# Optimization experiments

Measured on AMD Instinct MI355X. Metric: run time of the kernel, lower is better.

Reference implementation:

```python
import jax, jax.numpy as jnp
import numpy as np

N = 50000      # nodes
E = 800000     # edges
D = 128        # in_channels
H = 128        # hidden_channels
G = 64         # graphs in batch
OUT = 10       # out_channels
L = 6          # gcn layers (hardcoded in module)
EPS = 1e-5     # batchnorm eps


def setup_inputs() -> dict:
    key = jax.random.key(0)
    ks = jax.random.split(key, 8)
    s = 1.0 / np.sqrt(H)
    return {
        "x": jax.random.normal(ks[0], (N, D), jnp.float32),
        "edge_index": jax.random.randint(ks[1], (2, E), 0, N),
        "batch": jnp.sort(jax.random.randint(ks[2], (N,), 0, G)),
        "conv_W": jax.random.normal(ks[3], (L, D, H), jnp.float32) * s,
        "conv_b": jnp.zeros((L, H), jnp.float32),
        "bn_gamma": jnp.ones((L - 1, H), jnp.float32),
        "bn_beta": jnp.zeros((L - 1, H), jnp.float32),
        "head_W1": jax.random.normal(ks[4], (H, H), jnp.float32) * s,
        "head_b1": jnp.zeros((H,), jnp.float32),
        "head_bn_gamma": jnp.ones((H,), jnp.float32),
        "head_bn_beta": jnp.zeros((H,), jnp.float32),
        "head_W2": jax.random.normal(ks[5], (H, H), jnp.float32) * s,
        "head_b2": jnp.zeros((H,), jnp.float32),
        "head_W3": jax.random.normal(ks[6], (H, OUT), jnp.float32) * s,
        "head_b3": jnp.zeros((OUT,), jnp.float32),
    }


def _batchnorm(h, gamma, beta):
    # track_running_stats=False -> always batch statistics, biased variance
    mu = h.mean(axis=0)
    var = jnp.mean((h - mu) ** 2, axis=0)
    return (h - mu) * jax.lax.rsqrt(var + EPS) * gamma + beta


def reference(x, edge_index, batch, conv_W, conv_b, bn_gamma, bn_beta,
              head_W1, head_b1, head_bn_gamma, head_bn_beta,
              head_W2, head_b2, head_W3, head_b3):
    src, dst = edge_index[0], edge_index[1]
    # GCN symmetric norm with self-loops: deg = in-degree + 1
    deg = jnp.zeros((N,), x.dtype).at[dst].add(1.0) + 1.0
    dinv = jax.lax.rsqrt(deg)                 # deg^{-1/2}
    enorm = (dinv[src] * dinv[dst])[:, None]  # [E,1] edge weights
    self_w = (dinv * dinv)[:, None]           # [N,1] self-loop weight = 1/deg

    h = x
    for i in range(L):
        h = h @ conv_W[i]                                     # [N,H]
        agg = jnp.zeros_like(h).at[dst].add(h[src] * enorm)   # scatter-add
        h = agg + h * self_w + conv_b[i]
        if i < L - 1:
            h = jax.nn.relu(_batchnorm(h, bn_gamma[i], bn_beta[i]))
            # dropout(p=0.1) -> identity in eval

    # global_mean_pool over graphs
    counts = jnp.zeros((G,), h.dtype).at[batch].add(1.0)
    pooled = jnp.zeros((G, H), h.dtype).at[batch].add(h)
    pooled = pooled / jnp.clip(counts, 1.0)[:, None]

    # prediction head: Linear -> BN -> ReLU -> (Dropout) -> Linear -> ReLU -> Linear
    z = pooled @ head_W1 + head_b1
    z = jax.nn.relu(_batchnorm(z, head_bn_gamma, head_bn_beta))
    z = jax.nn.relu(z @ head_W2 + head_b2)
    return z @ head_W3 + head_b3
```

## Files before the change

### kernel.cpp

```cpp
#include <hip/hip_runtime.h>

#define N 50000
#define E 800000
#define H 128
#define G 64
#define OUTC 10
#define L 6
#define EPS 1e-5f
#define SLOTS 64

typedef unsigned short ushort_t;
typedef __attribute__((ext_vector_type(8))) short short8;
typedef __attribute__((ext_vector_type(8))) unsigned short ushort8;
typedef __attribute__((ext_vector_type(4))) float floatx4;

__device__ __forceinline__ void atomAddF(float* p, float v) {
  unsafeAtomicAdd(p, v);
}

__device__ __forceinline__ unsigned short f2bf(float f) {
  unsigned u = __float_as_uint(f);
  unsigned r = (u + 0x7FFF + ((u >> 16) & 1)) >> 16;
  return (unsigned short)r;
}
__device__ __forceinline__ float bf2f(unsigned short b) {
  return __uint_as_float(((unsigned)b) << 16);
}

__global__ void zero_kernel(int* __restrict__ p, int n) {
  int i = blockIdx.x * blockDim.x + threadIdx.x;
  if (i < n) p[i] = 0;
}

__global__ void csr_fill_kernel(const int* __restrict__ src, const int* __restrict__ dst,
                                int* __restrict__ cnt, int* __restrict__ csr) {
  int e = blockIdx.x * blockDim.x + threadIdx.x;
  if (e < E) {
    int d = dst[e];
    int pos = atomicAdd(&cnt[d], 1);
    if (pos < SLOTS) csr[(d << 6) + pos] = src[e];
  }
}

__global__ void dinv_kernel(const int* __restrict__ cnt, float* __restrict__ dinv) {
  int n = blockIdx.x * blockDim.x + threadIdx.x;
  if (n < N) dinv[n] = rsqrtf((float)(cnt[n] + 1));
}

__global__ void prep_kernel(const float* __restrict__ convW, ushort_t* __restrict__ WT) {
  int j = blockIdx.x * 256 + threadIdx.x;
  if (j < L * H * H) {
    int l = j >> 14, r = j & 16383;
    int n = r >> 7, k = r & 127;
    WT[j] = f2bf(convW[l * 16384 + k * 128 + n]);
  }
}

__global__ void cnt_kernel(const int* __restrict__ batch, float* __restrict__ cntg) {
  __shared__ int lb[G + 1];
  int t = threadIdx.x;
  if (t <= G) {
    int lo = 0, hi = N;
    while (lo < hi) { int m = (lo + hi) >> 1; if (batch[m] < t) lo = m + 1; else hi = m; }
    lb[t] = lo;
  }
  __syncthreads();
  if (t < G) cntg[t] = (float)(lb[t + 1] - lb[t]);
}

__global__ __launch_bounds__(256) void gemm_mfma_kernel(
    const ushort_t* __restrict__ Ab, const float* __restrict__ Af,
    const ushort_t* __restrict__ WT,
    const float* __restrict__ dinv, ushort_t* __restrict__ hWs,
    const float* __restrict__ bnsums, const float* __restrict__ gamma,
    const float* __restrict__ beta)
{
  const int tid = threadIdx.x;
  const int wave = tid >> 6, lane = tid & 63;
  const int quad = lane >> 4, m = lane & 15;
  const int row0 = blockIdx.x * 64 + wave * 16;
  const int arow = min(row0 + m, N - 1);
  const float invN = 1.0f / (float)N;

  short8 afrag[4];
  if (Af) {
#pragma unroll
    for (int kc = 0; kc < 4; ++kc) {
      const float* p = &Af[arow * H + kc * 32 + quad * 8];
      float4 f0 = *(const float4*)p;
      float4 f1 = *(const float4*)(p + 4);
      short8 a;
      a[0] = (short)f2bf(f0.x); a[1] = (short)f2bf(f0.y);
      a[2] = (short)f2bf(f0.z); a[3] = (short)f2bf(f0.w);
      a[4] = (short)f2bf(f1.x); a[5] = (short)f2bf(f1.y);
      a[6] = (short)f2bf(f1.z); a[7] = (short)f2bf(f1.w);
      afrag[kc] = a;
    }
  } else {
#pragma unroll
    for (int kc = 0; kc < 4; ++kc) {
      ushort8 raw = *(const ushort8*)&Ab[arow * H + kc * 32 + quad * 8];
      if (bnsums) {
        const int k0 = kc * 32 + quad * 8;
#pragma unroll
        for (int j = 0; j < 8; ++j) {
          float s = bnsums[k0 + j], q = bnsums[128 + k0 + j];
          float mu = s * invN;
          float var = q * invN - mu * mu;
          float rs = rsqrtf(var + EPS);
          float sc = gamma[k0 + j] * rs;
          float sh = beta[k0 + j] - mu * sc;
          raw[j] = f2bf(fmaxf(bf2f(raw[j]) * sc + sh, 0.f));
        }
      }
      short8 a;
#pragma unroll
      for (int j = 0; j < 8; ++j) a[j] = (short)raw[j];
      afrag[kc] = a;
    }
  }

  float dv[4];
#pragma unroll
  for (int i = 0; i < 4; ++i) {
    int r = row0 + quad * 4 + i;
    dv[i] = (r < N) ? dinv[r] : 0.f;
  }

  const short* WTs = (const short*)WT;
#pragma unroll
  for (int nt = 0; nt < 8; ++nt) {
    floatx4 acc = {0.f, 0.f, 0.f, 0.f};
#pragma unroll
    for (int kc = 0; kc < 4; ++kc) {
      short8 bfrag = *(const short8*)&WTs[(nt * 16 + m) * H + kc * 32 + quad * 8];
      acc = __builtin_amdgcn_mfma_f32_16x16x32_bf16(afrag[kc], bfrag, acc, 0, 0, 0);
    }
    int col = nt * 16 + m;
#pragma unroll
    for (int i = 0; i < 4; ++i) {
      int r = row0 + quad * 4 + i;
      if (r < N) hWs[r * H + col] = f2bf(acc[i] * dv[i]);
    }
  }
}

__global__ __launch_bounds__(256) void gather_kernel(
    const ushort_t* __restrict__ hWs, const int* __restrict__ csr,
    const int* __restrict__ cnt, const float* __restrict__ dinv,
    const float* __restrict__ bias, ushort_t* __restrict__ aggb)
{
  int t = blockIdx.x * 256 + threadIdx.x;
  int n = t >> 4, c8 = (t & 15) * 8;

  ushort8 us = *(const ushort8*)&hWs[n * H + c8];
  float acc[8];
#pragma unroll
  for (int j = 0; j < 8; ++j) acc[j] = bf2f(us[j]);

  int e = n << 6;
  int end = e + min(cnt[n], SLOTS);
  for (; e + 3 < end; e += 4) {
    int s0 = csr[e], s1 = csr[e + 1], s2 = csr[e + 2], s3 = csr[e + 3];
    ushort8 u0 = *(const ushort8*)&hWs[s0 * H + c8];
    ushort8 u1 = *(const ushort8*)&hWs[s1 * H + c8];
    ushort8 u2 = *(const ushort8*)&hWs[s2 * H + c8];
    ushort8 u3 = *(const ushort8*)&hWs[s3 * H + c8];
#pragma unroll
    for (int j = 0; j < 8; ++j)
      acc[j] += (bf2f(u0[j]) + bf2f(u1[j])) + (bf2f(u2[j]) + bf2f(u3[j]));
  }
  for (; e < end; ++e) {
    int s0 = csr[e];
    ushort8 u0 = *(const ushort8*)&hWs[s0 * H + c8];
#pragma unroll
    for (int j = 0; j < 8; ++j) acc[j] += bf2f(u0[j]);
  }

  float dn = dinv[n];
  float4 b0 = *(const float4*)&bias[c8];
  float4 b1 = *(const float4*)&bias[c8 + 4];
  float bb[8] = {b0.x, b0.y, b0.z, b0.w, b1.x, b1.y, b1.z, b1.w};
  ushort8 o;
#pragma unroll
  for (int j = 0; j < 8; ++j) o[j] = f2bf(acc[j] * dn + bb[j]);
  *(ushort8*)&aggb[n * H + c8] = o;
}

__global__ __launch_bounds__(256) void bn_stats_kernel(
    const ushort_t* __restrict__ a, float* __restrict__ sums)
{
  __shared__ float red[256];
  int tid = threadIdx.x;
  int c = tid & 127, half = tid >> 7;
  int r0 = blockIdx.x * 128;
  float s = 0.f, q = 0.f;
  for (int i = 0; i < 64; ++i) {
    int r = r0 + i * 2 + half;
    if (r < N) { float v = bf2f(a[r * H + c]); s += v; q += v * v; }
  }
  red[tid] = s; __syncthreads();
  float s2 = (half == 0) ? s + red[tid + 128] : 0.f;
  __syncthreads();
  red[tid] = q; __syncthreads();
  if (half == 0) {
    float q2 = q + red[tid + 128];
    atomAddF(&sums[c], s2);
    atomAddF(&sums[128 + c], q2);
  }
}

__global__ __launch_bounds__(256) void pool_kernel(
    const ushort_t* __restrict__ h, const int* __restrict__ batch,
    float* __restrict__ pooled )
{
  int r0 = blockIdx.x * 128;
  int rend = min(r0 + 128, N);
  int c = threadIdx.x & 127, half = threadIdx.x >> 7;
  float acc = 0.f;
  int curg = -1;
  for (int r = r0 + half; r < rend; r += 2) {
    int g = batch[r];
    if (g != curg) {
      if (curg >= 0) atomAddF(&pooled[curg * H + c], acc);
      acc = 0.f; curg = g;
    }
    acc += bf2f(h[r * H + c]);
  }
  if (curg >= 0) atomAddF(&pooled[curg * H + c], acc);
}

__global__ void head1_kernel(const float* __restrict__ pooled, const float* __restrict__ cntg,
                             const float* __restrict__ W1, const float* __restrict__ b1,
                             float* __restrict__ z1)
{
  int t = blockIdx.x * 256 + threadIdx.x;
  int g = t >> 7, c = t & 127;
  float s = 0.f;
  for (int k = 0; k < H; ++k) s += pooled[g * H + k] * W1[k * H + c];
  z1[t] = s / fmaxf(cntg[g], 1.0f) + b1[c];
}

__global__ void head_bn_kernel(float* __restrict__ z1,
                               const float* __restrict__ gamma, const float* __restrict__ beta)
{
  int c = threadIdx.x;
  float s = 0.f, q = 0.f;
  for (int g = 0; g < G; ++g) { float v = z1[g * H + c]; s += v; q += v * v; }
  float mu = s / (float)G;
  float var = q / (float)G - mu * mu;
  float rs = rsqrtf(var + EPS);
  float ga = gamma[c], be = beta[c];
  for (int g = 0; g < G; ++g) {
    float v = z1[g * H + c];
    z1[g * H + c] = fmaxf((v - mu) * rs * ga + be, 0.f);
  }
}

__global__ void head2_kernel(const float* __restrict__ z1, const float* __restrict__ W2,
                             const float* __restrict__ b2, float* __restrict__ z2)
{
  int t = blockIdx.x * 256 + threadIdx.x;
  int g = t >> 7, c = t & 127;
  float s = b2[c];
  for (int k = 0; k < H; ++k) s += z1[g * H + k] * W2[k * H + c];
  z2[t] = fmaxf(s, 0.f);
}

__global__ void head3_kernel(const float* __restrict__ z2, const float* __restrict__ W3,
                             const float* __restrict__ b3, float* __restrict__ out)
{
  int t = blockIdx.x * 256 + threadIdx.x;
  if (t < G * OUTC) {
    int g = t / OUTC, o = t % OUTC;
    float s = b3[o];
    for (int k = 0; k < H; ++k) s += z2[g * H + k] * W3[k * OUTC + o];
    out[t] = s;
  }
}

extern "C" void kernel_launch(void* const* d_in, const int* in_sizes, int n_in,
                              void* d_out, int out_size, void* d_ws, size_t ws_size,
                              hipStream_t stream) {
  const float* x     = (const float*)d_in[0];
  const int*   ei    = (const int*)d_in[1];
  const int*   srcp  = ei;
  const int*   dstp  = ei + E;
  const int*   batch = (const int*)d_in[2];
  const float* convW = (const float*)d_in[3];
  const float* convb = (const float*)d_in[4];
  const float* bng   = (const float*)d_in[5];
  const float* bnb   = (const float*)d_in[6];
  const float* W1    = (const float*)d_in[7];
  const float* b1    = (const float*)d_in[8];
  const float* hg    = (const float*)d_in[9];
  const float* hb    = (const float*)d_in[10];
  const float* W2    = (const float*)d_in[11];
  const float* b2    = (const float*)d_in[12];
  const float* W3    = (const float*)d_in[13];
  const float* b3    = (const float*)d_in[14];
  float* out = (float*)d_out;

  const size_t NH2 = (size_t)N * H / 2;
  float*    ws     = (float*)d_ws;
  ushort_t* aggb   = (ushort_t*)ws;
  ushort_t* hWs    = (ushort_t*)(ws + NH2);
  ushort_t* WT     = (ushort_t*)(ws + 2 * NH2);
  float*    dinv   = ws + 2 * NH2 + (L * H * H / 2);
  int*      csr    = (int*)(dinv + N);
  int*      cnt    = csr + (size_t)N * SLOTS;
  float*    bnsums = (float*)(cnt + N);
  float*    pooled = bnsums + (L - 1) * 256;
  float*    cntg   = pooled + G * H;
  float*    z1     = cntg + G;
  float*    z2     = z1 + G * H;

  const int zero_words = N + (L - 1) * 256 + G * H;
  zero_kernel<<<(zero_words + 255) / 256, 256, 0, stream>>>(cnt, zero_words);
  csr_fill_kernel<<<(E + 255) / 256, 256, 0, stream>>>(srcp, dstp, cnt, csr);
  dinv_kernel<<<(N + 255) / 256, 256, 0, stream>>>(cnt, dinv);
  cnt_kernel<<<1, 128, 0, stream>>>(batch, cntg);
  prep_kernel<<<(L * H * H + 255) / 256, 256, 0, stream>>>(convW, WT);

  for (int l = 0; l < L; ++l) {
    const ushort_t* Ab = (l == 0) ? nullptr : aggb;
    const float*    Af = (l == 0) ? x : nullptr;
    const float* bs = (l == 0) ? nullptr : bnsums + (l - 1) * 256;
    const float* ga = (l == 0) ? nullptr : bng + (size_t)(l - 1) * H;
    const float* be = (l == 0) ? nullptr : bnb + (size_t)(l - 1) * H;
    gemm_mfma_kernel<<<(N + 63) / 64, 256, 0, stream>>>(
        Ab, Af, WT + (size_t)l * H * H, dinv, hWs, bs, ga, be);
    gather_kernel<<<N * 16 / 256, 256, 0, stream>>>(
        hWs, csr, cnt, dinv, convb + (size_t)l * H, aggb);
    if (l < L - 1)
      bn_stats_kernel<<<(N + 127) / 128, 256, 0, stream>>>(aggb, bnsums + l * 256);
  }

  pool_kernel<<<(N + 127) / 128, 256, 0, stream>>>(aggb, batch, pooled);
  head1_kernel<<<32, 256, 0, stream>>>(pooled, cntg, W1, b1, z1);
  head_bn_kernel<<<1, 128, 0, stream>>>(z1, hg, hb);
  head2_kernel<<<32, 256, 0, stream>>>(z1, W2, b2, z2);
  head3_kernel<<<3, 256, 0, stream>>>(z2, W3, b3, out);
}
```

Measured before the change: 655.3 us.

## Store CSR indices as 16-bit, unroll gather by 8, vectorize BN stats

Neighbor indices are stored as unsigned 16-bit values, halving the CSR footprint, and the gather reads eight at once with a single vector load, issuing eight row fetches per iteration for more memory-level parallelism. The BN statistics kernel now reads 8 bf16 values per thread with vector loads and reduces across lanes with wave shuffles before a small shared-memory reduction. The 16-bit index cannot represent node ids above 65535; N is 50000 so it fits, but the scheme is tied to that size.

```diff
diff --git a/kernel.cpp b/kernel.cpp
--- a/kernel.cpp
+++ b/kernel.cpp
@@ -33,12 +33,12 @@
 }
 
 __global__ void csr_fill_kernel(const int* __restrict__ src, const int* __restrict__ dst,
-                                int* __restrict__ cnt, int* __restrict__ csr) {
+                                int* __restrict__ cnt, ushort_t* __restrict__ csru) {
   int e = blockIdx.x * blockDim.x + threadIdx.x;
   if (e < E) {
     int d = dst[e];
     int pos = atomicAdd(&cnt[d], 1);
-    if (pos < SLOTS) csr[(d << 6) + pos] = src[e];
+    if (pos < SLOTS) csru[(d << 6) + pos] = (ushort_t)src[e];
   }
 }
 
@@ -146,7 +146,7 @@
 }
 
 __global__ __launch_bounds__(256) void gather_kernel(
-    const ushort_t* __restrict__ hWs, const int* __restrict__ csr,
+    const ushort_t* __restrict__ hWs, const ushort_t* __restrict__ csru,
     const int* __restrict__ cnt, const float* __restrict__ dinv,
     const float* __restrict__ bias, ushort_t* __restrict__ aggb)
 {
@@ -158,20 +158,26 @@
 #pragma unroll
   for (int j = 0; j < 8; ++j) acc[j] = bf2f(us[j]);
 
-  int e = n << 6;
-  int end = e + min(cnt[n], SLOTS);
-  for (; e + 3 < end; e += 4) {
-    int s0 = csr[e], s1 = csr[e + 1], s2 = csr[e + 2], s3 = csr[e + 3];
-    ushort8 u0 = *(const ushort8*)&hWs[s0 * H + c8];
-    ushort8 u1 = *(const ushort8*)&hWs[s1 * H + c8];
-    ushort8 u2 = *(const ushort8*)&hWs[s2 * H + c8];
-    ushort8 u3 = *(const ushort8*)&hWs[s3 * H + c8];
+  const int base = n << 6;
+  const int deg = min(cnt[n], SLOTS);
+  int e = 0;
+  for (; e + 8 <= deg; e += 8) {
+    ushort8 idx = *(const ushort8*)&csru[base + e];
+    ushort8 u0 = *(const ushort8*)&hWs[(int)idx[0] * H + c8];
+    ushort8 u1 = *(const ushort8*)&hWs[(int)idx[1] * H + c8];
+    ushort8 u2 = *(const ushort8*)&hWs[(int)idx[2] * H + c8];
+    ushort8 u3 = *(const ushort8*)&hWs[(int)idx[3] * H + c8];
+    ushort8 u4 = *(const ushort8*)&hWs[(int)idx[4] * H + c8];
+    ushort8 u5 = *(const ushort8*)&hWs[(int)idx[5] * H + c8];
+    ushort8 u6 = *(const ushort8*)&hWs[(int)idx[6] * H + c8];
+    ushort8 u7 = *(const ushort8*)&hWs[(int)idx[7] * H + c8];
 #pragma unroll
     for (int j = 0; j < 8; ++j)
-      acc[j] += (bf2f(u0[j]) + bf2f(u1[j])) + (bf2f(u2[j]) + bf2f(u3[j]));
-  }
-  for (; e < end; ++e) {
-    int s0 = csr[e];
+      acc[j] += ((bf2f(u0[j]) + bf2f(u1[j])) + (bf2f(u2[j]) + bf2f(u3[j]))) +
+                ((bf2f(u4[j]) + bf2f(u5[j])) + (bf2f(u6[j]) + bf2f(u7[j])));
+  }
+  for (; e < deg; ++e) {
+    int s0 = csru[base + e];
     ushort8 u0 = *(const ushort8*)&hWs[s0 * H + c8];
 #pragma unroll
     for (int j = 0; j < 8; ++j) acc[j] += bf2f(u0[j]);
@@ -190,23 +196,44 @@
 __global__ __launch_bounds__(256) void bn_stats_kernel(
     const ushort_t* __restrict__ a, float* __restrict__ sums)
 {
-  __shared__ float red[256];
+  __shared__ float redS[4 * 128], redQ[4 * 128];
   int tid = threadIdx.x;
-  int c = tid & 127, half = tid >> 7;
+  int cg = tid & 15, nn = tid >> 4;
+  int c8 = cg * 8;
   int r0 = blockIdx.x * 128;
-  float s = 0.f, q = 0.f;
-  for (int i = 0; i < 64; ++i) {
-    int r = r0 + i * 2 + half;
-    if (r < N) { float v = bf2f(a[r * H + c]); s += v; q += v * v; }
-  }
-  red[tid] = s; __syncthreads();
-  float s2 = (half == 0) ? s + red[tid + 128] : 0.f;
+  float s[8], q[8];
+#pragma unroll
+  for (int j = 0; j < 8; ++j) { s[j] = 0.f; q[j] = 0.f; }
+#pragma unroll
+  for (int i = 0; i < 8; ++i) {
+    int r = r0 + i * 16 + nn;
+    if (r < N) {
+      ushort8 u = *(const ushort8*)&a[r * H + c8];
+#pragma unroll
+      for (int j = 0; j < 8; ++j) { float v = bf2f(u[j]); s[j] += v; q[j] += v * v; }
+    }
+  }
+  int wave = tid >> 6, lane = tid & 63;
+#pragma unroll
+  for (int j = 0; j < 8; ++j) {
+    s[j] += __shfl_xor(s[j], 16); s[j] += __shfl_xor(s[j], 32);
+    q[j] += __shfl_xor(q[j], 16); q[j] += __shfl_xor(q[j], 32);
+  }
+  if (lane < 16) {
+#pragma unroll
+    for (int j = 0; j < 8; ++j) {
+      redS[wave * 128 + lane * 8 + j] = s[j];
+      redQ[wave * 128 + lane * 8 + j] = q[j];
+    }
+  }
   __syncthreads();
-  red[tid] = q; __syncthreads();
-  if (half == 0) {
-    float q2 = q + red[tid + 128];
-    atomAddF(&sums[c], s2);
-    atomAddF(&sums[128 + c], q2);
+  if (tid < 128) {
+    float v = redS[tid] + redS[128 + tid] + redS[256 + tid] + redS[384 + tid];
+    atomAddF(&sums[tid], v);
+  } else {
+    int t2 = tid - 128;
+    float v = redQ[t2] + redQ[128 + t2] + redQ[256 + t2] + redQ[384 + t2];
+    atomAddF(&sums[128 + t2], v);
   }
 }
 
@@ -307,8 +334,8 @@
   ushort_t* hWs    = (ushort_t*)(ws + NH2);
   ushort_t* WT     = (ushort_t*)(ws + 2 * NH2);
   float*    dinv   = ws + 2 * NH2 + (L * H * H / 2);
-  int*      csr    = (int*)(dinv + N);
-  int*      cnt    = csr + (size_t)N * SLOTS;
+  ushort_t* csru   = (ushort_t*)(dinv + N);
+  int*      cnt    = (int*)(csru + (size_t)N * SLOTS);
   float*    bnsums = (float*)(cnt + N);
   float*    pooled = bnsums + (L - 1) * 256;
   float*    cntg   = pooled + G * H;
@@ -317,7 +344,7 @@
 
   const int zero_words = N + (L - 1) * 256 + G * H;
   zero_kernel<<<(zero_words + 255) / 256, 256, 0, stream>>>(cnt, zero_words);
-  csr_fill_kernel<<<(E + 255) / 256, 256, 0, stream>>>(srcp, dstp, cnt, csr);
+  csr_fill_kernel<<<(E + 255) / 256, 256, 0, stream>>>(srcp, dstp, cnt, csru);
   dinv_kernel<<<(N + 255) / 256, 256, 0, stream>>>(cnt, dinv);
   cnt_kernel<<<1, 128, 0, stream>>>(batch, cntg);
   prep_kernel<<<(L * H * H + 255) / 256, 256, 0, stream>>>(convW, WT);
@@ -331,7 +358,7 @@
     gemm_mfma_kernel<<<(N + 63) / 64, 256, 0, stream>>>(
         Ab, Af, WT + (size_t)l * H * H, dinv, hWs, bs, ga, be);
     gather_kernel<<<N * 16 / 256, 256, 0, stream>>>(
-        hWs, csr, cnt, dinv, convb + (size_t)l * H, aggb);
+        hWs, csru, cnt, dinv, convb + (size_t)l * H, aggb);
     if (l < L - 1)
       bn_stats_kernel<<<(N + 127) / 128, 256, 0, stream>>>(aggb, bnsums + l * 256);
   }
```

After: 618.2 us. -5.7%, faster.
